# Performance work log

Measured on AMD Instinct MI355X. Metric: run time of the kernel, lower is better.

The kernel has to match this reference:

```python
import jax, jax.numpy as jnp
import numpy as np

NMODELS, SZ_IN, SZ_OUT, B = 128, 256, 256, 4096

def setup_inputs() -> dict:
    key = jax.random.key(0)
    k1, k2, k3, k4 = jax.random.split(key, 4)
    inp = jax.random.normal(k1, (B, SZ_IN), dtype=jnp.float32)
    agent_ids = jax.random.randint(k2, (B,), 0, NMODELS, dtype=jnp.int32)
    # Embedding tables (init ~ N(0,1) like nn.Embedding default)
    weight_lut = jax.random.normal(k3, (NMODELS, SZ_IN * SZ_OUT), dtype=jnp.float32)
    bias_lut = jax.random.normal(k4, (NMODELS, SZ_OUT), dtype=jnp.float32)
    return {"inp": inp, "agent_ids": agent_ids, "weight_lut": weight_lut, "bias_lut": bias_lut}

def reference(inp, agent_ids, weight_lut, bias_lut):
    # per-id weight gather -> [B, sz_in, sz_out]
    W = weight_lut[agent_ids].reshape(-1, SZ_IN, SZ_OUT)
    b = bias_lut[agent_ids]  # [B, sz_out]
    out = jnp.einsum('bi,bio->bo', inp, W) + b
    return out
```

## Files before the change

### kernel.cpp

```cpp
#include <hip/hip_runtime.h>

#define NMODELS 128
#define SZ_IN 256
#define SZ_OUT 256
#define CHUNK 16
#define MAXLIST 192
#define LDSK 264

typedef __attribute__((ext_vector_type(4))) float f32x4;
typedef __attribute__((ext_vector_type(8))) short bf16x8;
typedef __attribute__((ext_vector_type(4))) short s16x4;

__device__ __forceinline__ short f2bf(float f) {
  union { float f; unsigned u; } v;
  v.f = f;
  const unsigned r = v.u + 0x7FFFu + ((v.u >> 16) & 1u);
  return (short)(r >> 16);
}

__global__ __launch_bounds__(256, 2) void linmulti_v10(
    const float* __restrict__ inp, const int* __restrict__ ids,
    const float* __restrict__ wlut, const float* __restrict__ blut,
    float* __restrict__ out, int B) {
  const int cq = blockIdx.x;
  const int m = blockIdx.y;
  const int tid = threadIdx.x;
  const int lane = tid & 63;
  const int wv = tid >> 6;
  const int q = lane >> 4;
  const int n16 = lane & 15;
  const int col = cq * 64 + wv * 16 + n16;

  const float* __restrict__ Wcol = wlut + (size_t)m * (SZ_IN * SZ_OUT) + col;
  float wraw[8][8];
#pragma unroll
  for (int kb = 0; kb < 8; ++kb)
#pragma unroll
    for (int j = 0; j < 8; ++j)
      wraw[kb][j] = Wcol[(size_t)(kb * 32 + q * 8 + j) * SZ_OUT];
  bf16x8 bfr[8];
#pragma unroll
  for (int kb = 0; kb < 8; ++kb)
#pragma unroll
    for (int j = 0; j < 8; ++j) bfr[kb][j] = f2bf(wraw[kb][j]);

  __shared__ int list[MAXLIST];
  __shared__ int wcnt[16][4];
  __shared__ short As[CHUNK * LDSK];

  int myid[16];
#pragma unroll
  for (int v = 0; v < 16; ++v) {
    const int b = v * 256 + tid;
    myid[v] = (b < B) ? ids[b] : -1;
  }
#pragma unroll
  for (int v = 0; v < 16; ++v) {
    const unsigned long long mk = __ballot(myid[v] == m);
    if (lane == 0) wcnt[v][wv] = __popcll(mk);
  }
  __syncthreads();
  int run = 0;
#pragma unroll
  for (int v = 0; v < 16; ++v) {
    int wbase = run;
    for (int w = 0; w < wv; ++w) wbase += wcnt[v][w];
    const unsigned long long mk = __ballot(myid[v] == m);
    if (myid[v] == m) {
      const int p = wbase + __popcll(mk & ((1ULL << lane) - 1ULL));
      if (p < MAXLIST) list[p] = v * 256 + tid;
    }
    for (int w = 0; w < 4; ++w) run += wcnt[v][w];
  }
  __syncthreads();
  const int cnt = (run < MAXLIST) ? run : MAXLIST;
  if (cnt == 0) return;

  const float bias_c = blut[m * SZ_OUT + col];

  const int nchunk = (cnt + CHUNK - 1) / CHUNK;
  for (int c = 0; c < nchunk; ++c) {
    const int s0 = c * CHUNK;
    if (c) __syncthreads();
#pragma unroll
    for (int v = 0; v < 4; ++v) {
      const int e4 = v * 256 + tid;
      const int s = e4 >> 6, f4 = e4 & 63;
      int p = s0 + s;
      if (p > cnt - 1) p = cnt - 1;
      const f32x4 a = ((const f32x4*)(inp + (size_t)list[p] * SZ_IN))[f4];
      s16x4 h;
#pragma unroll
      for (int j = 0; j < 4; ++j) h[j] = f2bf(a[j]);
      *(s16x4*)(As + s * LDSK + f4 * 4) = h;
    }
    __syncthreads();

    f32x4 acc = (f32x4){0.f, 0.f, 0.f, 0.f};
#pragma unroll
    for (int kb = 0; kb < 8; ++kb) {
      const bf16x8 afr = *(const bf16x8*)(As + n16 * LDSK + kb * 32 + q * 8);
      acc = __builtin_amdgcn_mfma_f32_16x16x32_bf16(afr, bfr[kb], acc, 0, 0, 0);
    }

#pragma unroll
    for (int r = 0; r < 4; ++r) {
      const int srow = q * 4 + r;
      if (s0 + srow < cnt)
        out[(size_t)list[s0 + srow] * SZ_OUT + col] = acc[r] + bias_c;
    }
  }
}

extern "C" void kernel_launch(void* const* d_in, const int* in_sizes, int n_in,
                              void* d_out, int out_size, void* d_ws, size_t ws_size,
                              hipStream_t stream) {
  const float* inp = (const float*)d_in[0];
  const int* ids = (const int*)d_in[1];
  const float* wlut = (const float*)d_in[2];
  const float* blut = (const float*)d_in[3];
  float* out = (float*)d_out;
  const int B = in_sizes[1];

  linmulti_v10<<<dim3(4, NMODELS), 256, 0, stream>>>(inp, ids, wlut, blut, out, B);
}
```

Baseline: 89.47 us.

## Split K across two wave groups with 512-thread blocks and LDS reduction

Doubles the block to 512 threads and splits the K dimension between two groups of four waves. Each wave now loads and converts half as many weight values, and the per-chunk MFMA chain is half as long. Partial sums are combined through shared memory before the output is written. The id-list scan is moved ahead of the bf16 conversion so the ids load overlaps with the weight loads. This adds an extra barrier and LDS traffic per chunk, and the 512-thread blocks may change how many blocks fit on each CU.

```diff
diff --git a/kernel.cpp b/kernel.cpp
--- a/kernel.cpp
+++ b/kernel.cpp
@@ -6,6 +6,7 @@
 #define CHUNK 16
 #define MAXLIST 192
 #define LDSK 264
+#define NT 512
 
 typedef __attribute__((ext_vector_type(4))) float f32x4;
 typedef __attribute__((ext_vector_type(8))) short bf16x8;
@@ -18,7 +19,7 @@
   return (short)(r >> 16);
 }
 
-__global__ __launch_bounds__(256, 2) void linmulti_v10(
+__global__ __launch_bounds__(NT, 2) void linmulti_v11(
     const float* __restrict__ inp, const int* __restrict__ ids,
     const float* __restrict__ wlut, const float* __restrict__ blut,
     float* __restrict__ out, int B) {
@@ -27,51 +28,58 @@
   const int tid = threadIdx.x;
   const int lane = tid & 63;
   const int wv = tid >> 6;
+  const int nt = wv & 3;
+  const int kh = wv >> 2;
   const int q = lane >> 4;
   const int n16 = lane & 15;
-  const int col = cq * 64 + wv * 16 + n16;
+  const int col = cq * 64 + nt * 16 + n16;
+  const int kbase = kh * 128;
+
+  __shared__ int list[MAXLIST];
+  __shared__ int wcnt[8][8];
+  __shared__ short As[CHUNK * LDSK];
+  __shared__ float red[4 * 256];
+
+  int myid[8];
+#pragma unroll
+  for (int v = 0; v < 8; ++v) {
+    const int b = v * NT + tid;
+    myid[v] = (b < B) ? ids[b] : -1;
+  }
 
   const float* __restrict__ Wcol = wlut + (size_t)m * (SZ_IN * SZ_OUT) + col;
-  float wraw[8][8];
+  float wraw[4][8];
 #pragma unroll
-  for (int kb = 0; kb < 8; ++kb)
+  for (int kb = 0; kb < 4; ++kb)
 #pragma unroll
     for (int j = 0; j < 8; ++j)
-      wraw[kb][j] = Wcol[(size_t)(kb * 32 + q * 8 + j) * SZ_OUT];
-  bf16x8 bfr[8];
+      wraw[kb][j] = Wcol[(size_t)(kbase + kb * 32 + q * 8 + j) * SZ_OUT];
+
 #pragma unroll
-  for (int kb = 0; kb < 8; ++kb)
-#pragma unroll
-    for (int j = 0; j < 8; ++j) bfr[kb][j] = f2bf(wraw[kb][j]);
-
-  __shared__ int list[MAXLIST];
-  __shared__ int wcnt[16][4];
-  __shared__ short As[CHUNK * LDSK];
-
-  int myid[16];
-#pragma unroll
-  for (int v = 0; v < 16; ++v) {
-    const int b = v * 256 + tid;
-    myid[v] = (b < B) ? ids[b] : -1;
-  }
-#pragma unroll
-  for (int v = 0; v < 16; ++v) {
+  for (int v = 0; v < 8; ++v) {
     const unsigned long long mk = __ballot(myid[v] == m);
     if (lane == 0) wcnt[v][wv] = __popcll(mk);
   }
   __syncthreads();
   int run = 0;
 #pragma unroll
-  for (int v = 0; v < 16; ++v) {
+  for (int v = 0; v < 8; ++v) {
     int wbase = run;
     for (int w = 0; w < wv; ++w) wbase += wcnt[v][w];
     const unsigned long long mk = __ballot(myid[v] == m);
     if (myid[v] == m) {
       const int p = wbase + __popcll(mk & ((1ULL << lane) - 1ULL));
-      if (p < MAXLIST) list[p] = v * 256 + tid;
+      if (p < MAXLIST) list[p] = v * NT + tid;
     }
-    for (int w = 0; w < 4; ++w) run += wcnt[v][w];
+    for (int w = 0; w < 8; ++w) run += wcnt[v][w];
   }
+
+  bf16x8 bfr[4];
+#pragma unroll
+  for (int kb = 0; kb < 4; ++kb)
+#pragma unroll
+    for (int j = 0; j < 8; ++j) bfr[kb][j] = f2bf(wraw[kb][j]);
+
   __syncthreads();
   const int cnt = (run < MAXLIST) ? run : MAXLIST;
   if (cnt == 0) return;
@@ -83,8 +91,8 @@
     const int s0 = c * CHUNK;
     if (c) __syncthreads();
 #pragma unroll
-    for (int v = 0; v < 4; ++v) {
-      const int e4 = v * 256 + tid;
+    for (int v = 0; v < 2; ++v) {
+      const int e4 = v * NT + tid;
       const int s = e4 >> 6, f4 = e4 & 63;
       int p = s0 + s;
       if (p > cnt - 1) p = cnt - 1;
@@ -98,16 +106,26 @@
 
     f32x4 acc = (f32x4){0.f, 0.f, 0.f, 0.f};
 #pragma unroll
-    for (int kb = 0; kb < 8; ++kb) {
-      const bf16x8 afr = *(const bf16x8*)(As + n16 * LDSK + kb * 32 + q * 8);
+    for (int kb = 0; kb < 4; ++kb) {
+      const bf16x8 afr =
+          *(const bf16x8*)(As + n16 * LDSK + kbase + kb * 32 + q * 8);
       acc = __builtin_amdgcn_mfma_f32_16x16x32_bf16(afr, bfr[kb], acc, 0, 0, 0);
     }
 
+    if (kh == 1) {
 #pragma unroll
-    for (int r = 0; r < 4; ++r) {
-      const int srow = q * 4 + r;
-      if (s0 + srow < cnt)
-        out[(size_t)list[s0 + srow] * SZ_OUT + col] = acc[r] + bias_c;
+      for (int r = 0; r < 4; ++r) red[nt * 256 + (q * 4 + r) * 16 + n16] = acc[r];
+    }
+    __syncthreads();
+    if (kh == 0) {
+#pragma unroll
+      for (int r = 0; r < 4; ++r) {
+        const int srow = q * 4 + r;
+        if (s0 + srow < cnt) {
+          out[(size_t)list[s0 + srow] * SZ_OUT + col] =
+              acc[r] + red[nt * 256 + (q * 4 + r) * 16 + n16] + bias_c;
+        }
+      }
     }
   }
 }
@@ -122,5 +140,5 @@
   float* out = (float*)d_out;
   const int B = in_sizes[1];
 
-  linmulti_v10<<<dim3(4, NMODELS), 256, 0, stream>>>(inp, ids, wlut, blut, out, B);
+  linmulti_v11<<<dim3(4, NMODELS), NT, 0, stream>>>(inp, ids, wlut, blut, out, B);
 }
```

Result: no change. 87.98 us (-1.7%).

## Load weights with coalesced float4 reads and reshuffle into MFMA fragments via LDS

Applied to the files above, without the earlier changes.

Weights were previously read as strided scalar column loads straight into MFMA fragment registers. They are now fetched as row-contiguous float4 loads, converted to bf16, scattered into an LDS staging buffer in fragment order, and read back as 16-byte fragment loads. The block grows to 512 threads covering 128 columns, so the grid halves and the id scan uses fewer iterations per thread. This adds an LDS round trip and an extra barrier, and the larger LDS footprint and register count could lower occupancy.

```diff
diff --git a/kernel.cpp b/kernel.cpp
--- a/kernel.cpp
+++ b/kernel.cpp
@@ -6,6 +6,8 @@
 #define CHUNK 16
 #define MAXLIST 192
 #define LDSK 264
+#define NT 512
+#define FRAGSTRIDE 520
 
 typedef __attribute__((ext_vector_type(4))) float f32x4;
 typedef __attribute__((ext_vector_type(8))) short bf16x8;
@@ -18,61 +20,83 @@
   return (short)(r >> 16);
 }
 
-__global__ __launch_bounds__(256, 2) void linmulti_v10(
+__global__ __launch_bounds__(NT, 2) void linmulti_v12(
     const float* __restrict__ inp, const int* __restrict__ ids,
     const float* __restrict__ wlut, const float* __restrict__ blut,
     float* __restrict__ out, int B) {
-  const int cq = blockIdx.x;
+  const int ch = blockIdx.x;
   const int m = blockIdx.y;
   const int tid = threadIdx.x;
   const int lane = tid & 63;
   const int wv = tid >> 6;
   const int q = lane >> 4;
   const int n16 = lane & 15;
-  const int col = cq * 64 + wv * 16 + n16;
+  const int col = ch * 128 + wv * 16 + n16;
 
-  const float* __restrict__ Wcol = wlut + (size_t)m * (SZ_IN * SZ_OUT) + col;
-  float wraw[8][8];
+  __shared__ short Wfrag[64 * FRAGSTRIDE];
+  __shared__ int list[MAXLIST];
+  __shared__ int wcnt[8][8];
+  short* As = Wfrag;
+
+  int myid[8];
 #pragma unroll
-  for (int kb = 0; kb < 8; ++kb)
-#pragma unroll
-    for (int j = 0; j < 8; ++j)
-      wraw[kb][j] = Wcol[(size_t)(kb * 32 + q * 8 + j) * SZ_OUT];
-  bf16x8 bfr[8];
-#pragma unroll
-  for (int kb = 0; kb < 8; ++kb)
-#pragma unroll
-    for (int j = 0; j < 8; ++j) bfr[kb][j] = f2bf(wraw[kb][j]);
+  for (int v = 0; v < 8; ++v) {
+    const int b = v * NT + tid;
+    myid[v] = (b < B) ? ids[b] : -1;
+  }
 
-  __shared__ int list[MAXLIST];
-  __shared__ int wcnt[16][4];
-  __shared__ short As[CHUNK * LDSK];
-
-  int myid[16];
+  const float* __restrict__ Wb = wlut + (size_t)m * (SZ_IN * SZ_OUT) + ch * 128;
+  f32x4 wraw[16];
 #pragma unroll
   for (int v = 0; v < 16; ++v) {
-    const int b = v * 256 + tid;
-    myid[v] = (b < B) ? ids[b] : -1;
+    const int e4 = v * NT + tid;
+    const int r = e4 >> 5;
+    const int c4 = e4 & 31;
+    wraw[v] = *(const f32x4*)(Wb + (size_t)r * SZ_OUT + c4 * 4);
   }
+
 #pragma unroll
-  for (int v = 0; v < 16; ++v) {
+  for (int v = 0; v < 8; ++v) {
     const unsigned long long mk = __ballot(myid[v] == m);
     if (lane == 0) wcnt[v][wv] = __popcll(mk);
   }
   __syncthreads();
   int run = 0;
 #pragma unroll
-  for (int v = 0; v < 16; ++v) {
+  for (int v = 0; v < 8; ++v) {
     int wbase = run;
     for (int w = 0; w < wv; ++w) wbase += wcnt[v][w];
     const unsigned long long mk = __ballot(myid[v] == m);
     if (myid[v] == m) {
       const int p = wbase + __popcll(mk & ((1ULL << lane) - 1ULL));
-      if (p < MAXLIST) list[p] = v * 256 + tid;
+      if (p < MAXLIST) list[p] = v * NT + tid;
     }
-    for (int w = 0; w < 4; ++w) run += wcnt[v][w];
+    for (int w = 0; w < 8; ++w) run += wcnt[v][w];
+  }
+
+#pragma unroll
+  for (int v = 0; v < 16; ++v) {
+    const int e4 = v * NT + tid;
+    const int r = e4 >> 5;
+    const int c0 = (e4 & 31) * 4;
+    const int kb = r >> 5;
+    const int qq = (r >> 3) & 3;
+    const int jj = r & 7;
+#pragma unroll
+    for (int e = 0; e < 4; ++e) {
+      const int c = c0 + e;
+      Wfrag[(kb * 8 + (c >> 4)) * FRAGSTRIDE + ((qq * 16) + (c & 15)) * 8 + jj] =
+          f2bf(wraw[v][e]);
+    }
   }
   __syncthreads();
+
+  bf16x8 bfr[8];
+#pragma unroll
+  for (int kb = 0; kb < 8; ++kb)
+    bfr[kb] = *(const bf16x8*)(Wfrag + (kb * 8 + wv) * FRAGSTRIDE + lane * 8);
+  __syncthreads();
+
   const int cnt = (run < MAXLIST) ? run : MAXLIST;
   if (cnt == 0) return;
 
@@ -83,8 +107,8 @@
     const int s0 = c * CHUNK;
     if (c) __syncthreads();
 #pragma unroll
-    for (int v = 0; v < 4; ++v) {
-      const int e4 = v * 256 + tid;
+    for (int v = 0; v < 2; ++v) {
+      const int e4 = v * NT + tid;
       const int s = e4 >> 6, f4 = e4 & 63;
       int p = s0 + s;
       if (p > cnt - 1) p = cnt - 1;
@@ -122,5 +146,5 @@
   float* out = (float*)d_out;
   const int B = in_sizes[1];
 
-  linmulti_v10<<<dim3(4, NMODELS), 256, 0, stream>>>(inp, ids, wlut, blut, out, B);
+  linmulti_v12<<<dim3(2, NMODELS), NT, 0, stream>>>(inp, ids, wlut, blut, out, B);
 }
```

Measured after the change: 87.82 us. Within noise of the previous version (-1.8%).
